# Kernel tuning notes

Measured on AMD Instinct MI355X. Metric: run time of the kernel, lower is better.

The kernel has to match this reference:

```python
import jax, jax.numpy as jnp
import numpy as np

N = 50000      # nodes per graph
E = 800000     # edges per graph (avg degree 16)
IN = 128       # in_channels == hidden_channels
HID = 128      # out_channels (heads=1)
R = 8          # num_relations
NEG = 0.2      # PyG RGATConv default negative_slope


def setup_inputs() -> dict:
    key = jax.random.key(0)
    ks = jax.random.split(key, 14)
    s_w = (2.0 / (IN + HID)) ** 0.5  # glorot-ish scale
    return {
        "x_one": jax.random.normal(ks[0], (N, IN), jnp.float32),
        "edge_index_one": jax.random.randint(ks[1], (2, E), 0, N),
        "edge_type_one": jax.random.randint(ks[2], (E,), 0, R),
        "x_two": jax.random.normal(ks[3], (N, IN), jnp.float32),
        "edge_index_two": jax.random.randint(ks[4], (2, E), 0, N),
        "edge_type_two": jax.random.randint(ks[5], (E,), 0, R),
        "W1": jax.random.normal(ks[6], (R, IN, HID), jnp.float32) * s_w,
        "q1": jax.random.normal(ks[7], (HID, 1), jnp.float32) * s_w,
        "k1": jax.random.normal(ks[8], (HID, 1), jnp.float32) * s_w,
        "b1": jnp.zeros((HID,), jnp.float32),
        "W2": jax.random.normal(ks[9], (R, IN, HID), jnp.float32) * s_w,
        "q2": jax.random.normal(ks[10], (HID, 1), jnp.float32) * s_w,
        "k2": jax.random.normal(ks[11], (HID, 1), jnp.float32) * s_w,
        "b2": jnp.zeros((HID,), jnp.float32),
    }


def _rgat(x, edge_index, edge_type, W, q, k, b):
    """PyG RGATConv (heads=1, additive-self-attention, across-relation)."""
    n = x.shape[0]
    src, dst = edge_index[0], edge_index[1]
    # per-relation linear transform of all nodes: [R, N, HID]
    xt = jnp.einsum('nd,rdo->rno', x, W)
    out_i = xt[edge_type, dst]   # [E, HID] transformed target (x_i W_r)
    out_j = xt[edge_type, src]   # [E, HID] transformed source (x_j W_r)
    qi = out_i @ q               # [E, 1]
    kj = out_j @ k               # [E, 1]
    alpha = jax.nn.leaky_relu(qi + kj, NEG)
    # scatter-softmax over incoming edges of each dst node
    amax = jax.ops.segment_max(alpha, dst, num_segments=n)
    amax = jnp.where(jnp.isfinite(amax), amax, 0.0)
    ex = jnp.exp(alpha - amax[dst])
    denom = jax.ops.segment_sum(ex, dst, num_segments=n) + 1e-16
    a = ex / denom[dst]          # [E, 1]
    # weighted scatter-add aggregation + bias
    out = jax.ops.segment_sum(a * out_j, dst, num_segments=n) + b
    return out


def reference(x_one, edge_index_one, edge_type_one,
              x_two, edge_index_two, edge_type_two,
              W1, q1, k1, b1, W2, q2, k2, b2):
    o1 = jax.nn.relu(_rgat(x_one, edge_index_one, edge_type_one, W1, q1, k1, b1))
    o2 = jax.nn.relu(_rgat(x_two, edge_index_two, edge_type_two, W2, q2, k2, b2))
    return (o1, o2)
```

## Files before the change

### kernel.cpp

```cpp
#include <hip/hip_runtime.h>


typedef unsigned short u16;
typedef __attribute__((ext_vector_type(8))) short short8;
typedef __attribute__((ext_vector_type(4))) float floatx4;
typedef __attribute__((ext_vector_type(4))) float float4v;

__device__ __forceinline__ u16 f2bf(float f) {
  union { float f; unsigned u; } v; v.f = f;
  unsigned r = v.u + 0x7FFFu + ((v.u >> 16) & 1u);
  return (u16)(r >> 16);
}
__device__ __forceinline__ float bflo(unsigned v) {
  union { unsigned u; float f; } c; c.u = v << 16; return c.f;
}
__device__ __forceinline__ float bfhi(unsigned v) {
  union { unsigned u; float f; } c; c.u = v & 0xffff0000u; return c.f;
}

__global__ void k_prep_wb(const float* __restrict__ W1, const float* __restrict__ W2,
                          u16* __restrict__ Wb, int KK) {
  int t = blockIdx.x * 256 + threadIdx.x;
  int lane = t & 63, nt = (t >> 6) & 7, kk = t >> 9;
  if (kk >= KK) return;
  const float* W = blockIdx.y ? W2 : W1;
  u16* out = Wb + (size_t)blockIdx.y * KK * 4096;
  int q = lane >> 4, m16 = lane & 15;
  int c = nt * 16 + m16;
  short8 v;
#pragma unroll
  for (int j = 0; j < 8; ++j) {
    int k = kk * 32 + q * 8 + j;
    v[j] = (short)f2bf(W[(size_t)k * 128 + c]);
  }
  *(short8*)(out + (size_t)t * 8) = v;
}

__global__ void k_prep_wqk(const float* __restrict__ W1, const float* __restrict__ q1,
                           const float* __restrict__ k1, const float* __restrict__ W2,
                           const float* __restrict__ q2, const float* __restrict__ k2,
                           float* __restrict__ Wq, float* __restrict__ Wk, int RD) {
  int wid = (blockIdx.x * 256 + threadIdx.x) >> 6;
  int lane = threadIdx.x & 63;
  if (wid >= 2 * RD) return;
  int g = wid >= RD;
  const float* W = g ? W2 : W1;
  const float* qv = g ? q2 : q1;
  const float* kv = g ? k2 : k1;
  const float* row = W + (size_t)(wid - g * RD) * 128;
  float a0 = row[lane], a1 = row[lane + 64];
  float vq = a0 * qv[lane] + a1 * qv[lane + 64];
  float vk = a0 * kv[lane] + a1 * kv[lane + 64];
#pragma unroll
  for (int off = 32; off; off >>= 1) {
    vq += __shfl_xor(vq, off);
    vk += __shfl_xor(vk, off);
  }
  if (lane == 0) { Wq[wid] = vq; Wk[wid] = vk; }
}

__global__ void k_prep_bqk(const float* __restrict__ Wq, const float* __restrict__ Wk,
                           u16* __restrict__ Bqk, int R) {
  int total = 2 * 4 * 64 * 8;
  for (int idx = threadIdx.x; idx < total; idx += 256) {
    int j = idx & 7, lane = (idx >> 3) & 63, kk = (idx >> 9) & 3, g = idx >> 11;
    int k = kk * 32 + ((lane >> 4) & 3) * 8 + j;
    int n = lane & 15;
    float v = (n < 8) ? Wq[(g * R + n) * 128 + k] : Wk[(g * R + (n & 7)) * 128 + k];
    Bqk[idx] = f2bf(v);
  }
}

__global__ void __launch_bounds__(256) k_sqk(
    const float* __restrict__ x1, const float* __restrict__ x2,
    const u16* __restrict__ Bqk, u16* __restrict__ xbf,
    float* __restrict__ sq, float* __restrict__ sk, int N) {
  int g = blockIdx.y;
  const float* x = g ? x2 : x1;
  u16* xb = xbf + (size_t)g * N * 128;
  int wave = threadIdx.x >> 6, lane = threadIdx.x & 63;
  int m0 = blockIdx.x * 64 + wave * 16;
  int q = lane >> 4, m16 = lane & 15;
  int node = m0 + m16;
  int srow = (node < N) ? node : N - 1;
  short8 bfrag[4];
#pragma unroll
  for (int kk = 0; kk < 4; ++kk) {
    const float* ap = x + (size_t)srow * 128 + kk * 32 + q * 8;
    float4v f0 = *(const float4v*)ap;
    float4v f1 = *(const float4v*)(ap + 4);
    short8 a;
    a[0] = (short)f2bf(f0.x); a[1] = (short)f2bf(f0.y);
    a[2] = (short)f2bf(f0.z); a[3] = (short)f2bf(f0.w);
    a[4] = (short)f2bf(f1.x); a[5] = (short)f2bf(f1.y);
    a[6] = (short)f2bf(f1.z); a[7] = (short)f2bf(f1.w);
    bfrag[kk] = a;
  }
  if (node < N) {
#pragma unroll
    for (int kk = 0; kk < 4; ++kk)
      *(short8*)(xb + (size_t)node * 128 + kk * 32 + q * 8) = bfrag[kk];
  }
  floatx4 accq = (floatx4){0.f, 0.f, 0.f, 0.f};
#pragma unroll
  for (int kk = 0; kk < 4; ++kk) {
    short8 aq = *(const short8*)(Bqk + ((size_t)g * 4 + kk) * 512 + lane * 8);
    accq = __builtin_amdgcn_mfma_f32_16x16x32_bf16(aq, bfrag[kk], accq, 0, 0, 0);
  }
  if (node < N) {
    float* dst = (q < 2 ? sq : sk) + (size_t)(g * N + node) * 8 + (q & 1) * 4;
    *(float4v*)dst = (float4v){accq[0], accq[1], accq[2], accq[3]};
  }
}

__global__ void __launch_bounds__(256) k_count(
    const int* __restrict__ d1, const int* __restrict__ d2,
    int* __restrict__ gcnt, int N, int E, int NB) {
  __shared__ int h[512];
  int tid = threadIdx.x;
  for (int i = tid; i < NB; i += 256) h[i] = 0;
  __syncthreads();
  int E2 = 2 * E;
  int e0 = blockIdx.x * 4096;
#pragma unroll
  for (int j = 0; j < 16; ++j) {
    int e = e0 + j * 256 + tid;
    if (e < E2) {
      int g = e >= E;
      int d = g ? d2[e - E] : d1[e];
      atomicAdd(&h[(g * N + d) >> 8], 1);
    }
  }
  __syncthreads();
  for (int i = tid; i < NB; i += 256)
    if (h[i]) atomicAdd(&gcnt[i], h[i]);
}

__global__ void k_bucket_scan(const int* __restrict__ gcnt, int* __restrict__ bbase,
                              int* __restrict__ bcur, int* __restrict__ offs,
                              int NB, int total, int N2) {
  __shared__ int sd[512];
  int tid = threadIdx.x;
  int v0 = (tid < NB) ? gcnt[tid] : 0;
  int v1 = (tid + 256 < NB) ? gcnt[tid + 256] : 0;
  sd[tid] = v0; sd[tid + 256] = v1;
  __syncthreads();
  for (int off = 1; off < 512; off <<= 1) {
    int t0 = (tid >= off) ? sd[tid - off] : 0;
    int t1 = (tid + 256 >= off) ? sd[tid + 256 - off] : 0;
    __syncthreads();
    sd[tid] += t0; sd[tid + 256] += t1;
    __syncthreads();
  }
  if (tid < NB) { int b = sd[tid] - v0; bbase[tid] = b; bcur[tid] = b; }
  if (tid + 256 < NB) { int b = sd[tid + 256] - v1; bbase[tid + 256] = b; bcur[tid + 256] = b; }
  if (tid == 0) { bbase[NB] = total; offs[N2] = total; }
}

__global__ void __launch_bounds__(256) k_bin(
    const int* __restrict__ ei1, const int* __restrict__ et1,
    const int* __restrict__ ei2, const int* __restrict__ et2,
    int* __restrict__ bcur, uint2* __restrict__ staged, int N, int E, int NB) {
  __shared__ int hist[512];
  __shared__ int basev[512];
  __shared__ int runstart[512];
  __shared__ unsigned sta[4096 * 2];
  int tid = threadIdx.x;
  int E2 = 2 * E;
  int e0 = blockIdx.x * 4096;
  int cnt2 = min(4096, E2 - e0);
  for (int i = tid; i < 512; i += 256) hist[i] = 0;
  __syncthreads();
  int dstg[16], srcet[16], rank[16];
#pragma unroll
  for (int j = 0; j < 16; ++j) {
    int e = e0 + j * 256 + tid;
    dstg[j] = -1;
    if (e < E2) {
      int g = e >= E;
      int el = e - (g ? E : 0);
      const int* ei = g ? ei2 : ei1;
      int s = ei[el], d = ei[E + el];
      int etv = (g ? et2 : et1)[el];
      dstg[j] = g * N + d;
      srcet[j] = (s << 3) | etv;
      rank[j] = atomicAdd(&hist[dstg[j] >> 8], 1);
    }
  }
  __syncthreads();
  basev[tid] = hist[tid];
  basev[tid + 256] = hist[tid + 256];
  __syncthreads();
  for (int off = 1; off < 512; off <<= 1) {
    int i0 = tid, i1 = tid + 256;
    int v0 = (i0 >= off) ? basev[i0 - off] : 0;
    int v1 = (i1 >= off) ? basev[i1 - off] : 0;
    __syncthreads();
    basev[i0] += v0; basev[i1] += v1;
    __syncthreads();
  }
  for (int i = tid; i < NB; i += 256)
    if (hist[i] > 0) runstart[i] = atomicAdd(&bcur[i], hist[i]);
  __syncthreads();
#pragma unroll
  for (int j = 0; j < 16; ++j)
    if (dstg[j] >= 0) {
      int b = dstg[j] >> 8;
      int slot = basev[b] - hist[b] + rank[j];
      sta[slot * 2] = (unsigned)dstg[j];
      sta[slot * 2 + 1] = (unsigned)srcet[j];
    }
  __syncthreads();
  for (int i = tid; i < cnt2; i += 256) {
    unsigned dg = sta[i * 2], se = sta[i * 2 + 1];
    int b = (int)(dg >> 8);
    int dest = runstart[b] + (i - (basev[b] - hist[b]));
    staged[dest] = make_uint2(dg, se);
  }
}

__global__ void __launch_bounds__(256) k_scatter2(
    const uint2* __restrict__ staged, const int* __restrict__ bbase,
    int* __restrict__ offs, int* __restrict__ csr, int N2) {
  __shared__ int hist[256];
  __shared__ int sd[256];
  __shared__ int cur[256];
  int b = blockIdx.x, tid = threadIdx.x;
  int nb0 = b << 8;
  int nnode = min(256, N2 - nb0);
  int s0 = bbase[b], s1 = bbase[b + 1];
  hist[tid] = 0;
  __syncthreads();
  for (int i = s0 + tid; i < s1; i += 256)
    atomicAdd(&hist[(int)staged[i].x - nb0], 1);
  __syncthreads();
  int v = hist[tid];
  sd[tid] = v; __syncthreads();
  for (int off = 1; off < 256; off <<= 1) {
    int t = (tid >= off) ? sd[tid - off] : 0;
    __syncthreads();
    sd[tid] += t;
    __syncthreads();
  }
  int ex = sd[tid] - v;
  if (tid < nnode) offs[nb0 + tid] = s0 + ex;
  cur[tid] = ex;
  __syncthreads();
  for (int i = s0 + tid; i < s1; i += 256) {
    uint2 en = staged[i];
    int node = (int)en.x - nb0;
    int sl = atomicAdd(&cur[node], 1);
    csr[s0 + sl] = (int)en.y;
  }
}

#define ACC8(RELE, W, V)                                              \
  {                                                                   \
    int _r = __builtin_amdgcn_readfirstlane(RELE) & 7;                \
    float _lo = bflo(V), _hi = bfhi(V);                               \
    switch (_r) {                                                     \
      case 0: y[0][0] += (W) * _lo; y[0][1] += (W) * _hi; break;      \
      case 1: y[1][0] += (W) * _lo; y[1][1] += (W) * _hi; break;      \
      case 2: y[2][0] += (W) * _lo; y[2][1] += (W) * _hi; break;      \
      case 3: y[3][0] += (W) * _lo; y[3][1] += (W) * _hi; break;      \
      case 4: y[4][0] += (W) * _lo; y[4][1] += (W) * _hi; break;      \
      case 5: y[5][0] += (W) * _lo; y[5][1] += (W) * _hi; break;      \
      case 6: y[6][0] += (W) * _lo; y[6][1] += (W) * _hi; break;      \
      default: y[7][0] += (W) * _lo; y[7][1] += (W) * _hi; break;     \
    }                                                                 \
  }

__global__ void __launch_bounds__(256) k_aggregate(
    const int* __restrict__ csr, const int* __restrict__ offs,
    const float* __restrict__ sq, const float* __restrict__ sk,
    const u16* __restrict__ xbf, const u16* __restrict__ Wb,
    const float* __restrict__ bias, float* __restrict__ out,
    int N, int node_base) {
  __shared__ u16 ylds[16][1032];
  int wave = threadIdx.x >> 6, lane = threadIdx.x & 63;
  int q = lane >> 4, m16 = lane & 15;
  const char* xbfb = (const char*)xbf;

  for (int t = 0; t < 4; ++t) {
    int nl = blockIdx.x * 16 + wave * 4 + t;
    float y[8][2] = {{0.f, 0.f}, {0.f, 0.f}, {0.f, 0.f}, {0.f, 0.f},
                     {0.f, 0.f}, {0.f, 0.f}, {0.f, 0.f}, {0.f, 0.f}};
    if (nl < N) {
      int node = node_base + nl;
      int start = offs[node], end = offs[node + 1];
      const float* sqn = sq + (size_t)node * 8;

      float al[8]; int pl[8];
      float m = -INFINITY;
      {
        int c = 0;
        for (int i = start + lane; i < end; i += 64, ++c) {
          int p = csr[i]; int s = p >> 3, e = p & 7;
          float a = sqn[e] + sk[(size_t)(node_base + s) * 8 + e];
          a = (a > 0.f) ? a : 0.2f * a;
          if (c < 8) { al[c] = a; pl[c] = p; }
          m = fmaxf(m, a);
        }
      }
#pragma unroll
      for (int off = 32; off; off >>= 1) m = fmaxf(m, __shfl_xor(m, off));

      float ssum = 0.f;
      {
        int c = 0;
        for (int i = start + lane; i < end; i += 64, ++c) {
          float a;
          if (c < 8) a = al[c];
          else {
            int p = csr[i]; int s = p >> 3, e = p & 7;
            a = sqn[e] + sk[(size_t)(node_base + s) * 8 + e];
            a = (a > 0.f) ? a : 0.2f * a;
          }
          ssum += __expf(a - m);
        }
      }
#pragma unroll
      for (int off = 32; off; off >>= 1) ssum += __shfl_xor(ssum, off);
      float inv = 1.f / (ssum + 1e-16f);

      int c = 0;
      for (int base = start; base < end; base += 64, ++c) {
        int cnt = min(64, end - base);
        float w = 0.f; int p = 0;
        {
          int i = base + lane;
          if (i < end) {
            float a;
            if (c < 8) { p = pl[c]; a = al[c]; }
            else {
              p = csr[i]; int s = p >> 3, e = p & 7;
              a = sqn[e] + sk[(size_t)(node_base + s) * 8 + e];
              a = (a > 0.f) ? a : 0.2f * a;
            }
            w = __expf(a - m) * inv;
          }
        }
        int j = 0;
        for (; j + 3 < cnt; j += 4) {
          float w0 = __shfl(w, j), w1 = __shfl(w, j + 1),
                w2 = __shfl(w, j + 2), w3 = __shfl(w, j + 3);
          int p0 = __shfl(p, j), p1 = __shfl(p, j + 1),
              p2 = __shfl(p, j + 2), p3 = __shfl(p, j + 3);
          unsigned v0 = *(const unsigned*)(xbfb + (((size_t)(unsigned)(p0 >> 3)) << 8) + lane * 4);
          unsigned v1 = *(const unsigned*)(xbfb + (((size_t)(unsigned)(p1 >> 3)) << 8) + lane * 4);
          unsigned v2 = *(const unsigned*)(xbfb + (((size_t)(unsigned)(p2 >> 3)) << 8) + lane * 4);
          unsigned v3 = *(const unsigned*)(xbfb + (((size_t)(unsigned)(p3 >> 3)) << 8) + lane * 4);
          ACC8(p0, w0, v0);
          ACC8(p1, w1, v1);
          ACC8(p2, w2, v2);
          ACC8(p3, w3, v3);
        }
        for (; j < cnt; ++j) {
          float w0 = __shfl(w, j);
          int p0 = __shfl(p, j);
          unsigned v0 = *(const unsigned*)(xbfb + (((size_t)(unsigned)(p0 >> 3)) << 8) + lane * 4);
          ACC8(p0, w0, v0);
        }
      }
    }
    int nrow = wave * 4 + t;
#pragma unroll
    for (int r = 0; r < 8; ++r) {
      unsigned pk = (unsigned)f2bf(y[r][0]) | ((unsigned)f2bf(y[r][1]) << 16);
      *(unsigned*)&ylds[nrow][r * 128 + lane * 2] = pk;
    }
  }
  __syncthreads();

  floatx4 acc0 = (floatx4){0.f, 0.f, 0.f, 0.f};
  floatx4 acc1 = (floatx4){0.f, 0.f, 0.f, 0.f};
  int nt0 = wave * 2, nt1 = wave * 2 + 1;
#pragma unroll
  for (int kk = 0; kk < 32; ++kk) {
    short8 b = *(const short8*)&ylds[m16][kk * 32 + q * 8];
    short8 a0 = *(const short8*)(Wb + ((size_t)(kk * 8 + nt0)) * 512 + lane * 8);
    short8 a1 = *(const short8*)(Wb + ((size_t)(kk * 8 + nt1)) * 512 + lane * 8);
    acc0 = __builtin_amdgcn_mfma_f32_16x16x32_bf16(a0, b, acc0, 0, 0, 0);
    acc1 = __builtin_amdgcn_mfma_f32_16x16x32_bf16(a1, b, acc1, 0, 0, 0);
  }
  int onode = blockIdx.x * 16 + m16;
  if (onode < N) {
    float* op = out + (size_t)onode * 128;
    int ch0 = nt0 * 16 + q * 4, ch1 = nt1 * 16 + q * 4;
    float4v bv0 = *(const float4v*)(bias + ch0);
    float4v bv1 = *(const float4v*)(bias + ch1);
    float4v o0 = (float4v){fmaxf(acc0[0] + bv0.x, 0.f), fmaxf(acc0[1] + bv0.y, 0.f),
                           fmaxf(acc0[2] + bv0.z, 0.f), fmaxf(acc0[3] + bv0.w, 0.f)};
    float4v o1 = (float4v){fmaxf(acc1[0] + bv1.x, 0.f), fmaxf(acc1[1] + bv1.y, 0.f),
                           fmaxf(acc1[2] + bv1.z, 0.f), fmaxf(acc1[3] + bv1.w, 0.f)};
    *(float4v*)(op + ch0) = o0;
    *(float4v*)(op + ch1) = o1;
  }
}

extern "C" void kernel_launch(void* const* d_in, const int* in_sizes, int n_in,
                              void* d_out, int out_size, void* d_ws, size_t ws_size,
                              hipStream_t stream) {
  const float* x1 = (const float*)d_in[0];
  const int* ei1 = (const int*)d_in[1];
  const int* et1 = (const int*)d_in[2];
  const float* x2 = (const float*)d_in[3];
  const int* ei2 = (const int*)d_in[4];
  const int* et2 = (const int*)d_in[5];
  const float* W1 = (const float*)d_in[6];
  const float* q1 = (const float*)d_in[7];
  const float* k1 = (const float*)d_in[8];
  const float* b1 = (const float*)d_in[9];
  const float* W2 = (const float*)d_in[10];
  const float* q2 = (const float*)d_in[11];
  const float* k2 = (const float*)d_in[12];
  const float* b2 = (const float*)d_in[13];

  const int N = in_sizes[0] / 128;
  const int E = in_sizes[1] / 2;
  const int R = in_sizes[6] / (128 * 128);
  const int KK = R * 4;
  const int N2 = 2 * N;
  const int NB = (N2 + 255) >> 8;

  size_t off = 0;
  char* w = (char*)d_ws;
  auto carve = [&](size_t bytes) -> void* {
    void* p = w + off;
    off += (bytes + 255) & ~(size_t)255;
    return p;
  };
  u16* Wb = (u16*)carve((size_t)2 * KK * 4096 * 2);
  u16* Bqk = (u16*)carve((size_t)2 * 4 * 64 * 8 * 2);
  float* Wq = (float*)carve((size_t)2 * R * 128 * 4);
  float* Wk = (float*)carve((size_t)2 * R * 128 * 4);
  u16* xbf = (u16*)carve((size_t)N2 * 128 * 2);
  float* sq = (float*)carve((size_t)N2 * 8 * 4);
  float* sk = (float*)carve((size_t)N2 * 8 * 4);
  int* offs = (int*)carve((size_t)(N2 + 1) * 4);
  int* gcnt = (int*)carve(512 * 4);
  int* bbase = (int*)carve(520 * 4);
  int* bcur = (int*)carve(512 * 4);
  uint2* staged = (uint2*)carve((size_t)2 * E * 8);
  int* csr = (int*)carve((size_t)2 * E * 4);
  if (off > ws_size) return;

  const int nbin = (2 * E + 4095) / 4096;

  hipMemsetAsync(gcnt, 0, 512 * 4, stream);
  k_prep_wb<<<dim3((KK * 512 + 255) / 256, 2), dim3(256), 0, stream>>>(W1, W2, Wb, KK);
  k_prep_wqk<<<dim3((2 * R * 128 * 64 + 255) / 256), dim3(256), 0, stream>>>(
      W1, q1, k1, W2, q2, k2, Wq, Wk, R * 128);
  k_prep_bqk<<<dim3(1), dim3(256), 0, stream>>>(Wq, Wk, Bqk, R);
  k_sqk<<<dim3((N + 63) / 64, 2), dim3(256), 0, stream>>>(x1, x2, Bqk, xbf, sq, sk, N);
  k_count<<<dim3(nbin), dim3(256), 0, stream>>>(ei1 + E, ei2 + E, gcnt, N, E, NB);
  k_bucket_scan<<<dim3(1), dim3(256), 0, stream>>>(gcnt, bbase, bcur, offs, NB, 2 * E, N2);
  k_bin<<<dim3(nbin), dim3(256), 0, stream>>>(ei1, et1, ei2, et2, bcur, staged, N, E, NB);
  k_scatter2<<<dim3(NB), dim3(256), 0, stream>>>(staged, bbase, offs, csr, N2);

  for (int g = 0; g < 2; ++g) {
    const float* bv = g ? b2 : b1;
    float* outp = (float*)d_out + (size_t)g * N * 128;
    k_aggregate<<<dim3((N + 15) / 16), dim3(256), 0, stream>>>(
        csr, offs, sq, sk, xbf + (size_t)g * N * 128, Wb + (size_t)g * KK * 4096,
        bv, outp, N, g * N);
  }
}
```

Measured before the change: 396.6 us.

## Accumulate per-relation sums in LDS via atomics and merge both graphs into one launch

Replaces the register-resident per-relation accumulators, which were selected through a wave-uniform switch, with fp32 LDS accumulation using unsafeAtomicAdd indexed by relation. The LDS tile is zeroed first and converted to bf16 with v_cvt_pk_bf16_f32 just before the MFMA projection. The two per-graph launches are folded into one grid, with the graph index derived from blockIdx. The aim is to remove branch overhead and register pressure and to save a launch, at the cost of LDS atomic traffic and a larger fp32 LDS footprint that may lower occupancy.

```diff
diff --git a/kernel.cpp b/kernel.cpp
--- a/kernel.cpp
+++ b/kernel.cpp
@@ -254,138 +254,138 @@
   }
 }
 
-#define ACC8(RELE, W, V)                                              \
-  {                                                                   \
-    int _r = __builtin_amdgcn_readfirstlane(RELE) & 7;                \
-    float _lo = bflo(V), _hi = bfhi(V);                               \
-    switch (_r) {                                                     \
-      case 0: y[0][0] += (W) * _lo; y[0][1] += (W) * _hi; break;      \
-      case 1: y[1][0] += (W) * _lo; y[1][1] += (W) * _hi; break;      \
-      case 2: y[2][0] += (W) * _lo; y[2][1] += (W) * _hi; break;      \
-      case 3: y[3][0] += (W) * _lo; y[3][1] += (W) * _hi; break;      \
-      case 4: y[4][0] += (W) * _lo; y[4][1] += (W) * _hi; break;      \
-      case 5: y[5][0] += (W) * _lo; y[5][1] += (W) * _hi; break;      \
-      case 6: y[6][0] += (W) * _lo; y[6][1] += (W) * _hi; break;      \
-      default: y[7][0] += (W) * _lo; y[7][1] += (W) * _hi; break;     \
-    }                                                                 \
-  }
-
 __global__ void __launch_bounds__(256) k_aggregate(
     const int* __restrict__ csr, const int* __restrict__ offs,
     const float* __restrict__ sq, const float* __restrict__ sk,
     const u16* __restrict__ xbf, const u16* __restrict__ Wb,
-    const float* __restrict__ bias, float* __restrict__ out,
-    int N, int node_base) {
-  __shared__ u16 ylds[16][1032];
+    const float* __restrict__ b1, const float* __restrict__ b2,
+    float* __restrict__ out, int N, int nbg, int KK) {
+  __shared__ __align__(16) float ylds[16 * 1028];
   int wave = threadIdx.x >> 6, lane = threadIdx.x & 63;
   int q = lane >> 4, m16 = lane & 15;
+  int g = blockIdx.x >= nbg;
+  int bl = blockIdx.x - (g ? nbg : 0);
+  size_t gN = (size_t)g * N;
   const char* xbfb = (const char*)xbf;
 
+  float4v z4 = (float4v){0.f, 0.f, 0.f, 0.f};
+  for (int i = threadIdx.x; i < 16 * 1028 / 4; i += 256)
+    *(float4v*)&ylds[i * 4] = z4;
+  __syncthreads();
+
   for (int t = 0; t < 4; ++t) {
-    int nl = blockIdx.x * 16 + wave * 4 + t;
-    float y[8][2] = {{0.f, 0.f}, {0.f, 0.f}, {0.f, 0.f}, {0.f, 0.f},
-                     {0.f, 0.f}, {0.f, 0.f}, {0.f, 0.f}, {0.f, 0.f}};
-    if (nl < N) {
-      int node = node_base + nl;
-      int start = offs[node], end = offs[node + 1];
-      const float* sqn = sq + (size_t)node * 8;
-
-      float al[8]; int pl[8];
-      float m = -INFINITY;
+    int nl = bl * 16 + wave * 4 + t;
+    if (nl >= N) continue;
+    int gnode = (int)gN + nl;
+    int start = offs[gnode], end = offs[gnode + 1];
+    const float* sqn = sq + (size_t)gnode * 8;
+    float* yrow = ylds + (wave * 4 + t) * 1028;
+
+    float al[8]; int pl[8];
+    float m = -INFINITY;
+    {
+      int c = 0;
+      for (int i = start + lane; i < end; i += 64, ++c) {
+        int p = csr[i]; int s = p >> 3, e = p & 7;
+        float a = sqn[e] + sk[(gN + s) * 8 + e];
+        a = (a > 0.f) ? a : 0.2f * a;
+        if (c < 8) { al[c] = a; pl[c] = p; }
+        m = fmaxf(m, a);
+      }
+    }
+#pragma unroll
+    for (int off = 32; off; off >>= 1) m = fmaxf(m, __shfl_xor(m, off));
+
+    float ssum = 0.f;
+    {
+      int c = 0;
+      for (int i = start + lane; i < end; i += 64, ++c) {
+        float a;
+        if (c < 8) a = al[c];
+        else {
+          int p = csr[i]; int s = p >> 3, e = p & 7;
+          a = sqn[e] + sk[(gN + s) * 8 + e];
+          a = (a > 0.f) ? a : 0.2f * a;
+        }
+        ssum += __expf(a - m);
+      }
+    }
+#pragma unroll
+    for (int off = 32; off; off >>= 1) ssum += __shfl_xor(ssum, off);
+    float inv = 1.f / (ssum + 1e-16f);
+
+    int c = 0;
+    for (int base = start; base < end; base += 64, ++c) {
+      int cnt = min(64, end - base);
+      float w = 0.f; int p = 0;
       {
-        int c = 0;
-        for (int i = start + lane; i < end; i += 64, ++c) {
-          int p = csr[i]; int s = p >> 3, e = p & 7;
-          float a = sqn[e] + sk[(size_t)(node_base + s) * 8 + e];
-          a = (a > 0.f) ? a : 0.2f * a;
-          if (c < 8) { al[c] = a; pl[c] = p; }
-          m = fmaxf(m, a);
+        int i = base + lane;
+        if (i < end) {
+          float a;
+          if (c < 8) { p = pl[c]; a = al[c]; }
+          else {
+            p = csr[i]; int s = p >> 3, e = p & 7;
+            a = sqn[e] + sk[(gN + s) * 8 + e];
+            a = (a > 0.f) ? a : 0.2f * a;
+          }
+          w = __expf(a - m) * inv;
         }
       }
-#pragma unroll
-      for (int off = 32; off; off >>= 1) m = fmaxf(m, __shfl_xor(m, off));
-
-      float ssum = 0.f;
-      {
-        int c = 0;
-        for (int i = start + lane; i < end; i += 64, ++c) {
-          float a;
-          if (c < 8) a = al[c];
-          else {
-            int p = csr[i]; int s = p >> 3, e = p & 7;
-            a = sqn[e] + sk[(size_t)(node_base + s) * 8 + e];
-            a = (a > 0.f) ? a : 0.2f * a;
-          }
-          ssum += __expf(a - m);
-        }
+      int j = 0;
+      for (; j + 3 < cnt; j += 4) {
+        float w0 = __shfl(w, j), w1 = __shfl(w, j + 1),
+              w2 = __shfl(w, j + 2), w3 = __shfl(w, j + 3);
+        int p0 = __shfl(p, j), p1 = __shfl(p, j + 1),
+            p2 = __shfl(p, j + 2), p3 = __shfl(p, j + 3);
+        unsigned v0 = *(const unsigned*)(xbfb + ((gN + (unsigned)(p0 >> 3)) << 8) + lane * 4);
+        unsigned v1 = *(const unsigned*)(xbfb + ((gN + (unsigned)(p1 >> 3)) << 8) + lane * 4);
+        unsigned v2 = *(const unsigned*)(xbfb + ((gN + (unsigned)(p2 >> 3)) << 8) + lane * 4);
+        unsigned v3 = *(const unsigned*)(xbfb + ((gN + (unsigned)(p3 >> 3)) << 8) + lane * 4);
+        float* a0 = yrow + (p0 & 7) * 128 + lane * 2;
+        float* a1 = yrow + (p1 & 7) * 128 + lane * 2;
+        float* a2 = yrow + (p2 & 7) * 128 + lane * 2;
+        float* a3 = yrow + (p3 & 7) * 128 + lane * 2;
+        unsafeAtomicAdd(a0, w0 * bflo(v0)); unsafeAtomicAdd(a0 + 1, w0 * bfhi(v0));
+        unsafeAtomicAdd(a1, w1 * bflo(v1)); unsafeAtomicAdd(a1 + 1, w1 * bfhi(v1));
+        unsafeAtomicAdd(a2, w2 * bflo(v2)); unsafeAtomicAdd(a2 + 1, w2 * bfhi(v2));
+        unsafeAtomicAdd(a3, w3 * bflo(v3)); unsafeAtomicAdd(a3 + 1, w3 * bfhi(v3));
       }
-#pragma unroll
-      for (int off = 32; off; off >>= 1) ssum += __shfl_xor(ssum, off);
-      float inv = 1.f / (ssum + 1e-16f);
-
-      int c = 0;
-      for (int base = start; base < end; base += 64, ++c) {
-        int cnt = min(64, end - base);
-        float w = 0.f; int p = 0;
-        {
-          int i = base + lane;
-          if (i < end) {
-            float a;
-            if (c < 8) { p = pl[c]; a = al[c]; }
-            else {
-              p = csr[i]; int s = p >> 3, e = p & 7;
-              a = sqn[e] + sk[(size_t)(node_base + s) * 8 + e];
-              a = (a > 0.f) ? a : 0.2f * a;
-            }
-            w = __expf(a - m) * inv;
-          }
-        }
-        int j = 0;
-        for (; j + 3 < cnt; j += 4) {
-          float w0 = __shfl(w, j), w1 = __shfl(w, j + 1),
-                w2 = __shfl(w, j + 2), w3 = __shfl(w, j + 3);
-          int p0 = __shfl(p, j), p1 = __shfl(p, j + 1),
-              p2 = __shfl(p, j + 2), p3 = __shfl(p, j + 3);
-          unsigned v0 = *(const unsigned*)(xbfb + (((size_t)(unsigned)(p0 >> 3)) << 8) + lane * 4);
-          unsigned v1 = *(const unsigned*)(xbfb + (((size_t)(unsigned)(p1 >> 3)) << 8) + lane * 4);
-          unsigned v2 = *(const unsigned*)(xbfb + (((size_t)(unsigned)(p2 >> 3)) << 8) + lane * 4);
-          unsigned v3 = *(const unsigned*)(xbfb + (((size_t)(unsigned)(p3 >> 3)) << 8) + lane * 4);
-          ACC8(p0, w0, v0);
-          ACC8(p1, w1, v1);
-          ACC8(p2, w2, v2);
-          ACC8(p3, w3, v3);
-        }
-        for (; j < cnt; ++j) {
-          float w0 = __shfl(w, j);
-          int p0 = __shfl(p, j);
-          unsigned v0 = *(const unsigned*)(xbfb + (((size_t)(unsigned)(p0 >> 3)) << 8) + lane * 4);
-          ACC8(p0, w0, v0);
-        }
+      for (; j < cnt; ++j) {
+        float w0 = __shfl(w, j);
+        int p0 = __shfl(p, j);
+        unsigned v0 = *(const unsigned*)(xbfb + ((gN + (unsigned)(p0 >> 3)) << 8) + lane * 4);
+        float* a0 = yrow + (p0 & 7) * 128 + lane * 2;
+        unsafeAtomicAdd(a0, w0 * bflo(v0)); unsafeAtomicAdd(a0 + 1, w0 * bfhi(v0));
       }
     }
-    int nrow = wave * 4 + t;
-#pragma unroll
-    for (int r = 0; r < 8; ++r) {
-      unsigned pk = (unsigned)f2bf(y[r][0]) | ((unsigned)f2bf(y[r][1]) << 16);
-      *(unsigned*)&ylds[nrow][r * 128 + lane * 2] = pk;
-    }
-  }
-  __syncthreads();
-
+  }
+  __syncthreads();
+
+  const u16* Wbg = Wb + (size_t)g * KK * 4096;
   floatx4 acc0 = (floatx4){0.f, 0.f, 0.f, 0.f};
   floatx4 acc1 = (floatx4){0.f, 0.f, 0.f, 0.f};
   int nt0 = wave * 2, nt1 = wave * 2 + 1;
+  const float* brow = ylds + m16 * 1028;
 #pragma unroll
   for (int kk = 0; kk < 32; ++kk) {
-    short8 b = *(const short8*)&ylds[m16][kk * 32 + q * 8];
-    short8 a0 = *(const short8*)(Wb + ((size_t)(kk * 8 + nt0)) * 512 + lane * 8);
-    short8 a1 = *(const short8*)(Wb + ((size_t)(kk * 8 + nt1)) * 512 + lane * 8);
-    acc0 = __builtin_amdgcn_mfma_f32_16x16x32_bf16(a0, b, acc0, 0, 0, 0);
-    acc1 = __builtin_amdgcn_mfma_f32_16x16x32_bf16(a1, b, acc1, 0, 0, 0);
-  }
-  int onode = blockIdx.x * 16 + m16;
-  if (onode < N) {
-    float* op = out + (size_t)onode * 128;
+    float4v f0 = *(const float4v*)(brow + kk * 32 + q * 8);
+    float4v f1 = *(const float4v*)(brow + kk * 32 + q * 8 + 4);
+    unsigned r0, r1, r2, r3;
+    asm("v_cvt_pk_bf16_f32 %0, %1, %2" : "=v"(r0) : "v"(f0.x), "v"(f0.y));
+    asm("v_cvt_pk_bf16_f32 %0, %1, %2" : "=v"(r1) : "v"(f0.z), "v"(f0.w));
+    asm("v_cvt_pk_bf16_f32 %0, %1, %2" : "=v"(r2) : "v"(f1.x), "v"(f1.y));
+    asm("v_cvt_pk_bf16_f32 %0, %1, %2" : "=v"(r3) : "v"(f1.z), "v"(f1.w));
+    union { unsigned u[4]; short8 s; } bb;
+    bb.u[0] = r0; bb.u[1] = r1; bb.u[2] = r2; bb.u[3] = r3;
+    short8 a0 = *(const short8*)(Wbg + ((size_t)(kk * 8 + nt0)) * 512 + lane * 8);
+    short8 a1 = *(const short8*)(Wbg + ((size_t)(kk * 8 + nt1)) * 512 + lane * 8);
+    acc0 = __builtin_amdgcn_mfma_f32_16x16x32_bf16(a0, bb.s, acc0, 0, 0, 0);
+    acc1 = __builtin_amdgcn_mfma_f32_16x16x32_bf16(a1, bb.s, acc1, 0, 0, 0);
+  }
+  int ln = bl * 16 + m16;
+  if (ln < N) {
+    const float* bias = g ? b2 : b1;
+    float* op = out + (gN + ln) * 128;
     int ch0 = nt0 * 16 + q * 4, ch1 = nt1 * 16 + q * 4;
     float4v bv0 = *(const float4v*)(bias + ch0);
     float4v bv1 = *(const float4v*)(bias + ch1);
@@ -446,6 +446,7 @@
   if (off > ws_size) return;
 
   const int nbin = (2 * E + 4095) / 4096;
+  const int nbg = (N + 15) / 16;
 
   hipMemsetAsync(gcnt, 0, 512 * 4, stream);
   k_prep_wb<<<dim3((KK * 512 + 255) / 256, 2), dim3(256), 0, stream>>>(W1, W2, Wb, KK);
@@ -458,11 +459,6 @@
   k_bin<<<dim3(nbin), dim3(256), 0, stream>>>(ei1, et1, ei2, et2, bcur, staged, N, E, NB);
   k_scatter2<<<dim3(NB), dim3(256), 0, stream>>>(staged, bbase, offs, csr, N2);
 
-  for (int g = 0; g < 2; ++g) {
-    const float* bv = g ? b2 : b1;
-    float* outp = (float*)d_out + (size_t)g * N * 128;
-    k_aggregate<<<dim3((N + 15) / 16), dim3(256), 0, stream>>>(
-        csr, offs, sq, sk, xbf + (size_t)g * N * 128, Wb + (size_t)g * KK * 4096,
-        bv, outp, N, g * N);
-  }
-}
+  k_aggregate<<<dim3(2 * nbg), dim3(256), 0, stream>>>(
+      csr, offs, sq, sk, xbf, Wb, b1, b2, (float*)d_out, N, nbg, KK);
+}
```

New measurement: 1.340 ms. +237.9%, slower.
